# Optimization experiments

Hardware: AMD Instinct MI355X
Metric: run time of the kernel (lower is better)

Reference implementation:

```python
import jax, jax.numpy as jnp
import numpy as np

T = 2048        # num tokens
HID = 2048      # hidden_size
HQ = 16         # num_heads
HKV = 8         # num_kv_heads
D = 128         # head_dim
P = 2           # power retention exponent
THETA = 10000.0 # rope base
SCALE = D ** -0.5


def setup_inputs() -> dict:
    key = jax.random.key(0)
    ks = jax.random.split(key, 8)
    s = 0.02
    return {
        "positions": jnp.arange(T, dtype=jnp.int64) if jax.config.jax_enable_x64 else jnp.arange(T, dtype=jnp.int32),
        "hidden_states": jax.random.normal(ks[0], (T, HID), jnp.float32),
        "Wq": jax.random.normal(ks[1], (HID, HQ * D), jnp.float32) * s,
        "bq": jnp.zeros((HQ * D,), jnp.float32),
        "Wk": jax.random.normal(ks[2], (HID, HKV * D), jnp.float32) * s,
        "bk": jnp.zeros((HKV * D,), jnp.float32),
        "Wv": jax.random.normal(ks[3], (HID, HKV * D), jnp.float32) * s,
        "bv": jnp.zeros((HKV * D,), jnp.float32),
        "Wg": jax.random.normal(ks[4], (HID, HKV), jnp.float32) * s,
        "bg": jnp.zeros((HKV,), jnp.float32),
        "Wo": jax.random.normal(ks[5], (HQ * D, HID), jnp.float32) * s,
        "bo": jnp.zeros((HID,), jnp.float32),
    }


def _rope_neox(x, pos):
    # x: [T, H, D], pos: [T]; rotate-half (neox) style, rotary_dim == head_dim
    half = D // 2
    inv_freq = 1.0 / (THETA ** (jnp.arange(0, D, 2, dtype=jnp.float32) / D))  # [D/2]
    freqs = pos.astype(jnp.float32)[:, None] * inv_freq                        # [T, D/2]
    cos = jnp.cos(freqs)[:, None, :]
    sin = jnp.sin(freqs)[:, None, :]
    x1, x2 = x[..., :half], x[..., half:]
    return jnp.concatenate([x1 * cos - x2 * sin, x2 * cos + x1 * sin], axis=-1)


def reference(positions, hidden_states, Wq, bq, Wk, bk, Wv, bv, Wg, bg, Wo, bo):
    # QKVG projections
    q = (hidden_states @ Wq + bq).reshape(T, HQ, D)
    k = (hidden_states @ Wk + bk).reshape(T, HKV, D)
    v = (hidden_states @ Wv + bv).reshape(T, HKV, D)
    g = hidden_states @ Wg + bg            # [T, HKV], one gate scalar per kv head

    # RoPE on q/k, logsigmoid gate in fp32
    q = _rope_neox(q, positions)
    k = _rope_neox(k, positions)
    g = jax.nn.log_sigmoid(g.astype(jnp.float32))   # [T, HKV], <= 0
    G = jnp.cumsum(g, axis=0)                       # [T, HKV] cumulative log-decay

    # GQA: expand kv heads to query heads
    rep = HQ // HKV
    k = jnp.repeat(k, rep, axis=1)   # [T, HQ, D]
    v = jnp.repeat(v, rep, axis=1)
    G = jnp.repeat(G, rep, axis=1)   # [T, HQ]

    # Power retention (quadratic attention form, seq_len <= switch_over_seq_len):
    # W_ij = (scale * q_i . k_j)^p * exp(G_i - G_j), causal j <= i
    S = jnp.einsum('thd,shd->hts', q, k) * SCALE      # [H, T, T]
    S = S ** P
    Gh = G.T                                          # [H, T]
    mask = jnp.tril(jnp.ones((T, T), dtype=bool))
    diff = jnp.where(mask[None], Gh[:, :, None] - Gh[:, None, :], -jnp.inf)
    W = S * jnp.exp(diff)                             # decay<=1 inside mask, 0 outside

    out = jnp.einsum('hts,shd->thd', W, v)            # [T, H, D]
    out = out.reshape(T, HQ * D) @ Wo + bo            # o_proj
    return out
```

## Files before the change

kernel.cpp:

```cpp
#include <hip/hip_runtime.h>
#include <hip/hip_bf16.h>
#include <math.h>

#define T_SEQ 2048
#define HID 2048
#define HQ 16
#define HKV 8
#define D_HEAD 128
#define HALF 64
#define SCALE_F 0.08838834764831845f
#define PROJW 4096

typedef __attribute__((ext_vector_type(8))) short bf16x8;
typedef __attribute__((ext_vector_type(4))) float f32x4;

static __device__ __forceinline__ short f2bf(float x) {
  unsigned u = __builtin_bit_cast(unsigned, x);
  unsigned r = (u + 0x7FFF + ((u >> 16) & 1)) >> 16;
  return (short)r;
}
static __device__ __forceinline__ float bf2f(unsigned short u) {
  unsigned v = ((unsigned)u) << 16;
  return __builtin_bit_cast(float, v);
}

#define GLDS(gsrc, ldst) \
  __builtin_amdgcn_global_load_lds((const __attribute__((address_space(1))) void*)(gsrc), \
                                   (__attribute__((address_space(3))) void*)(ldst), 16, 0, 0)

__global__ __launch_bounds__(256)
void cvt_bf16(const float* __restrict__ in, short* __restrict__ out, int n4)
{
  int i = blockIdx.x * blockDim.x + threadIdx.x;
  if (i >= n4) return;
  float4 v = reinterpret_cast<const float4*>(in)[i];
  short4 o;
  o.x = f2bf(v.x); o.y = f2bf(v.y); o.z = f2bf(v.z); o.w = f2bf(v.w);
  reinterpret_cast<short4*>(out)[i] = o;
}

__global__ __launch_bounds__(256)
void transpose_all(const float* __restrict__ Wq, const float* __restrict__ Wk,
                   const float* __restrict__ Wv, const float* __restrict__ Wo,
                   short* __restrict__ BTall, short* __restrict__ WoT)
{
  const int bx = blockIdx.x;
  const int k0 = blockIdx.y * 32;
  const float* src; short* dst; int Nsrc, n0;
  if (bx < 64)       { src = Wq; Nsrc = 2048; dst = BTall;                       n0 = bx * 32; }
  else if (bx < 96)  { src = Wk; Nsrc = 1024; dst = BTall + (size_t)2048 * 2048; n0 = (bx - 64) * 32; }
  else if (bx < 128) { src = Wv; Nsrc = 1024; dst = BTall + (size_t)3072 * 2048; n0 = (bx - 96) * 32; }
  else               { src = Wo; Nsrc = 2048; dst = WoT;                         n0 = (bx - 128) * 32; }

  __shared__ float tile[32][33];
  const int r = threadIdx.x >> 5, c = threadIdx.x & 31;
  #pragma unroll
  for (int i = 0; i < 4; ++i)
    tile[r + i * 8][c] = src[(size_t)(k0 + r + i * 8) * Nsrc + n0 + c];
  __syncthreads();
  const int n = threadIdx.x >> 3, k4 = (threadIdx.x & 7) * 4;
  short4 o;
  o.x = f2bf(tile[k4 + 0][n]); o.y = f2bf(tile[k4 + 1][n]);
  o.z = f2bf(tile[k4 + 2][n]); o.w = f2bf(tile[k4 + 3][n]);
  *reinterpret_cast<short4*>(&dst[(size_t)(n0 + n) * 2048 + k0 + k4]) = o;
}

__global__ __launch_bounds__(256)
void pack_bias(const float* __restrict__ bq, const float* __restrict__ bk,
               const float* __restrict__ bv, float* __restrict__ bcat)
{
  const int i = blockIdx.x * 256 + threadIdx.x;
  bcat[i] = (i < 2048) ? bq[i] : ((i < 3072) ? bk[i - 2048] : bv[i - 3072]);
}

template <bool OBF>
__global__ __launch_bounds__(256)
void gemm_bf16(const short* __restrict__ A, const short* __restrict__ BT,
               const float* __restrict__ bias, void* __restrict__ Cout,
               int N, int K)
{
  __shared__ short As[4][128 * 32];
  __shared__ short Bs[4][128 * 32];
  const int tid = threadIdx.x;
  const int wave = tid >> 6, lane = tid & 63;
  const int bm0 = blockIdx.y * 128, bn0 = blockIdx.x * 128;
  const int wm = (wave >> 1) * 64, wn = (wave & 1) * 64;

  const int srow = wave * 32 + (lane >> 2);
  const int scol = (lane & 3) * 8;
  const short* Abase = A + (size_t)(bm0 + srow) * K + scol;
  const short* Bbase = BT + (size_t)(bn0 + srow) * K + scol;

  f32x4 acc[4][4] = {};
  const int nk = K >> 5;

#define STAGE(buf, kk)                                                        \
  do {                                                                        \
    GLDS(Abase + ((kk) << 5), &As[buf][(wave * 32) * 32]);                    \
    GLDS(Abase + ((kk) << 5) + (size_t)16 * K, &As[buf][(wave * 32 + 16) * 32]); \
    GLDS(Bbase + ((kk) << 5), &Bs[buf][(wave * 32) * 32]);                    \
    GLDS(Bbase + ((kk) << 5) + (size_t)16 * K, &Bs[buf][(wave * 32 + 16) * 32]); \
  } while (0)

  STAGE(0, 0);
  STAGE(1, 1);
  asm volatile("s_waitcnt vmcnt(4)" ::: "memory");
  asm volatile("s_barrier" ::: "memory");
  __builtin_amdgcn_sched_barrier(0);

  const int kof = (lane >> 4) * 8;
  const int rA = wm + (lane & 15);
  const int rB = wn + (lane & 15);

  for (int t = 0; t < nk; ++t) {
    const int cur = t & 3;
    if (t + 2 < nk) STAGE((t + 2) & 3, t + 2);

    bf16x8 af[4], bfr[4];
    #pragma unroll
    for (int i = 0; i < 4; ++i) {
      af[i]  = *reinterpret_cast<const bf16x8*>(&As[cur][(rA + i * 16) * 32 + kof]);
      bfr[i] = *reinterpret_cast<const bf16x8*>(&Bs[cur][(rB + i * 16) * 32 + kof]);
    }
    #pragma unroll
    for (int i = 0; i < 4; ++i)
      #pragma unroll
      for (int j = 0; j < 4; ++j)
        acc[i][j] = __builtin_amdgcn_mfma_f32_16x16x32_bf16(af[i], bfr[j], acc[i][j], 0, 0, 0);

    if (t + 1 < nk) {
      if (t + 2 < nk) asm volatile("s_waitcnt vmcnt(4)" ::: "memory");
      else            asm volatile("s_waitcnt vmcnt(0)" ::: "memory");
      asm volatile("s_barrier" ::: "memory");
      __builtin_amdgcn_sched_barrier(0);
    }
  }

  const int crow = wm + (lane >> 4) * 4;
  const int ccol = wn + (lane & 15);
  #pragma unroll
  for (int j = 0; j < 4; ++j) {
    const int col = bn0 + ccol + j * 16;
    const float b = bias[col];
    #pragma unroll
    for (int i = 0; i < 4; ++i)
      #pragma unroll
      for (int r = 0; r < 4; ++r) {
        const int row = bm0 + crow + i * 16 + r;
        const float v = acc[i][j][r] + b;
        if constexpr (OBF)
          ((short*)Cout)[(size_t)row * N + col] = f2bf(v);
        else
          ((float*)Cout)[(size_t)row * N + col] = v;
      }
  }
#undef STAGE
}

__global__ __launch_bounds__(256)
void gproj_kernel(const float* __restrict__ hs, const float* __restrict__ Wg,
                  const float* __restrict__ bg, float* __restrict__ gT)
{
  const int t = blockIdx.x, tid = threadIdx.x;
  __shared__ float red[256][9];
  float a[8] = {0.f, 0.f, 0.f, 0.f, 0.f, 0.f, 0.f, 0.f};
  for (int cc = tid; cc < HID; cc += 256) {
    const float hv = hs[(size_t)t * HID + cc];
    const float4 w0 = *reinterpret_cast<const float4*>(Wg + (size_t)cc * 8);
    const float4 w1 = *reinterpret_cast<const float4*>(Wg + (size_t)cc * 8 + 4);
    a[0] = fmaf(hv, w0.x, a[0]); a[1] = fmaf(hv, w0.y, a[1]);
    a[2] = fmaf(hv, w0.z, a[2]); a[3] = fmaf(hv, w0.w, a[3]);
    a[4] = fmaf(hv, w1.x, a[4]); a[5] = fmaf(hv, w1.y, a[5]);
    a[6] = fmaf(hv, w1.z, a[6]); a[7] = fmaf(hv, w1.w, a[7]);
  }
  #pragma unroll
  for (int j = 0; j < 8; ++j) red[tid][j] = a[j];
  __syncthreads();
  for (int s = 128; s >= 1; s >>= 1) {
    if (tid < s) {
      #pragma unroll
      for (int j = 0; j < 8; ++j) red[tid][j] += red[tid + s][j];
    }
    __syncthreads();
  }
  if (tid < 8) {
    const float x = red[0][tid] + bg[tid];
    const float nx = -x;
    const float sp = (nx > 20.f) ? nx : log1pf(expf(nx));
    gT[(size_t)tid * T_SEQ + t] = -sp;
  }
}

__global__ __launch_bounds__(512)
void gscan_kernel(const float* __restrict__ gT, float* __restrict__ Gct)
{
  const int h = blockIdx.x;
  const int tid = threadIdx.x;
  const int wid = tid >> 6, lane = tid & 63;
  __shared__ float wsum[8];

  const float4 v = reinterpret_cast<const float4*>(gT + (size_t)h * T_SEQ)[tid];
  const float p0 = v.x, p1 = p0 + v.y, p2 = p1 + v.z, p3 = p2 + v.w;

  float sc = p3;
  #pragma unroll
  for (int off = 1; off < 64; off <<= 1) {
    const float o = __shfl_up(sc, off, 64);
    if (lane >= off) sc += o;
  }
  if (lane == 63) wsum[wid] = sc;
  __syncthreads();
  float wof = 0.f;
  #pragma unroll
  for (int w = 0; w < 8; ++w) wof += (w < wid) ? wsum[w] : 0.f;

  const float excl = wof + sc - p3;
  reinterpret_cast<float4*>(Gct + (size_t)h * T_SEQ)[tid] =
      make_float4(excl + p0, excl + p1, excl + p2, excl + p3);
}

__global__ __launch_bounds__(192)
void rope_kernel(short* __restrict__ proj)
{
  const int t = blockIdx.x;
  __shared__ float cs[64], sn[64];
  if (threadIdx.x < 64) {
    const int i = threadIdx.x;
    const float f = (float)t * powf(10000.0f, -(float)i / 64.0f);
    cs[i] = cosf(f); sn[i] = sinf(f);
  }
  __syncthreads();
  const int u = threadIdx.x;
  const int hh = u >> 3, ch = u & 7;
  short* base = proj + (size_t)t * PROJW +
                ((hh < HQ) ? hh * D_HEAD : 2048 + (hh - HQ) * D_HEAD);
  bf16x8 x1 = *reinterpret_cast<bf16x8*>(base + ch * 8);
  bf16x8 x2 = *reinterpret_cast<bf16x8*>(base + HALF + ch * 8);
  #pragma unroll
  for (int j = 0; j < 8; ++j) {
    const float a = bf2f((unsigned short)x1[j]);
    const float b = bf2f((unsigned short)x2[j]);
    const float cc = cs[ch * 8 + j], ss = sn[ch * 8 + j];
    x1[j] = f2bf(a * cc - b * ss);
    x2[j] = f2bf(b * cc + a * ss);
  }
  *reinterpret_cast<bf16x8*>(base + ch * 8) = x1;
  *reinterpret_cast<bf16x8*>(base + HALF + ch * 8) = x2;
}

__global__ __launch_bounds__(256)
void vtrans_kernel(const unsigned short* __restrict__ proj, unsigned short* __restrict__ vt)
{
  __shared__ unsigned short tile[32][33];
  const int tt = blockIdx.x * 32, dd = blockIdx.y * 32, hk = blockIdx.z;
  const int c = threadIdx.x & 31, r0 = (threadIdx.x >> 5) * 4;
  #pragma unroll
  for (int i = 0; i < 4; ++i)
    tile[r0 + i][c] = proj[(size_t)(tt + r0 + i) * PROJW + 3072 + hk * 128 + dd + c];
  __syncthreads();
  #pragma unroll
  for (int i = 0; i < 4; ++i)
    vt[(size_t)(hk * 128 + dd + r0 + i) * T_SEQ + tt + c] = tile[c][r0 + i];
}

__global__ __launch_bounds__(256, 1)
void attn_mfma(const short* __restrict__ proj, const short* __restrict__ vt,
               const float* __restrict__ Gct, short* __restrict__ outb)
{
  __shared__ __align__(16) char smem[86528];
  const int hk = blockIdx.x;
  const int tb = blockIdx.y * 64;
  const int tid = threadIdx.x;
  const int wid = tid >> 6, lane = tid & 63;
  const int c = lane & 15, g = lane >> 4;
  const int h = 2 * hk + (wid >> 1);
  const int tw = tb + (wid & 1) * 32;
  const float* Gh = Gct + (size_t)hk * T_SEQ;

  const float glim = Gh[tb] + 90.0f;
  int lo = 0, hi = tb;
  while (lo < hi) {
    const int mid = (lo + hi) >> 1;
    if (Gh[mid] > glim) lo = mid + 1; else hi = mid;
  }
  const int sfirst = lo & ~63;
  const int nst = ((tb - sfirst) >> 6) + 1;

  bf16x8 qf[2][4];
  #pragma unroll
  for (int tt = 0; tt < 2; ++tt)
    #pragma unroll
    for (int kb = 0; kb < 4; ++kb)
      qf[tt][kb] = *reinterpret_cast<const bf16x8*>(
          proj + (size_t)(tw + 16 * tt + c) * PROJW + h * D_HEAD + kb * 32 + g * 8);
  const float gt0 = Gh[tw + c];
  const float gt1 = Gh[tw + 16 + c];
  const float gtw = Gh[tw];
  const int twmax = tw + 31;

  f32x4 accv[2][8] = {};

#define ASTG(buf, s64)                                                                   \
  do {                                                                                   \
    _Pragma("unroll")                                                                    \
    for (int i2 = 0; i2 < 4; ++i2) {                                                     \
      const int cid = tid + 256 * i2;                                                    \
      const int kr = cid >> 4, kc = cid & 15;                                            \
      GLDS(proj + (size_t)((s64) + kr) * PROJW + 2048 + hk * 128 + ((kc ^ (kr & 7)) * 8),\
           smem + (buf) * 16384 + cid * 16);                                             \
      const int vr = cid >> 3, vc = cid & 7;                                             \
      GLDS(vt + (size_t)(hk * 128 + vr) * T_SEQ + (s64) + ((vc ^ (vr & 7)) * 8),         \
           smem + 32768 + (buf) * 16384 + cid * 16);                                     \
    }                                                                                    \
    if (tid < 64) ((float*)(smem + 86016))[(buf) * 64 + tid] = Gh[(s64) + tid];          \
  } while (0)

  ASTG(0, sfirst);
  __syncthreads();

  for (int i = 0; i < nst; ++i) {
    const int cur = i & 1;
    if (i + 1 < nst) ASTG(cur ^ 1, sfirst + (i + 1) * 64);
    const int sbase64 = sfirst + i * 64;
    const float* Gss = (const float*)(smem + 86016) + cur * 64;
    char* Pmy = smem + 65536 + wid * 5120;

    #pragma unroll
    for (int st = 0; st < 2; ++st) {
      const int s0 = sbase64 + st * 32;
      if (s0 > twmax) continue;
      if (gtw - Gss[st * 32 + 31] < -90.0f) continue;

      bf16x8 kf[2][4];
      #pragma unroll
      for (int sg = 0; sg < 2; ++sg)
        #pragma unroll
        for (int kb = 0; kb < 4; ++kb) {
          const int row = st * 32 + 16 * sg + c;
          const int byt = (row * 256 + kb * 64 + g * 16) ^ ((c & 7) << 4);
          kf[sg][kb] = *reinterpret_cast<const bf16x8*>(smem + cur * 16384 + byt);
        }
      f32x4 sa[2][2] = {};
      #pragma unroll
      for (int kb = 0; kb < 4; ++kb)
        #pragma unroll
        for (int sg = 0; sg < 2; ++sg)
          #pragma unroll
          for (int tt = 0; tt < 2; ++tt)
            sa[sg][tt] = __builtin_amdgcn_mfma_f32_16x16x32_bf16(
                kf[sg][kb], qf[tt][kb], sa[sg][tt], 0, 0, 0);

      #pragma unroll
      for (int sg = 0; sg < 2; ++sg) {
        const float4 gs = *reinterpret_cast<const float4*>(&Gss[st * 32 + sg * 16 + g * 4]);
        const float gsv[4] = {gs.x, gs.y, gs.z, gs.w};
        #pragma unroll
        for (int tt = 0; tt < 2; ++tt) {
          const int tg = tw + 16 * tt + c;
          const float gt = tt ? gt1 : gt0;
          const int sg0 = s0 + sg * 16 + g * 4;
          float w[4];
          #pragma unroll
          for (int r = 0; r < 4; ++r) {
            const float dv = sa[sg][tt][r] * SCALE_F;
            const float ww = dv * dv * __expf(gt - gsv[r]);
            w[r] = (sg0 + r <= tg) ? ww : 0.0f;
          }
          uint2 pv;
          pv.x = ((unsigned)(unsigned short)f2bf(w[1]) << 16) | (unsigned short)f2bf(w[0]);
          pv.y = ((unsigned)(unsigned short)f2bf(w[3]) << 16) | (unsigned short)f2bf(w[2]);
          *reinterpret_cast<uint2*>(Pmy + st * 2560 + (c + 16 * tt) * 80 + 8 * g + 32 * sg) = pv;
        }
      }
      asm volatile("s_waitcnt lgkmcnt(0)" ::: "memory");
      __builtin_amdgcn_sched_barrier(0);

      bf16x8 pf[2];
      #pragma unroll
      for (int tt = 0; tt < 2; ++tt)
        pf[tt] = *reinterpret_cast<const bf16x8*>(Pmy + st * 2560 + (c + 16 * tt) * 80 + g * 16);

      #pragma unroll
      for (int db = 0; db < 8; ++db) {
        const int row = 16 * db + c;
        const int byt = (row * 128 + st * 64 + g * 16) ^ ((c & 7) << 4);
        const bf16x8 vf = *reinterpret_cast<const bf16x8*>(smem + 32768 + cur * 16384 + byt);
        #pragma unroll
        for (int tt = 0; tt < 2; ++tt)
          accv[tt][db] = __builtin_amdgcn_mfma_f32_16x16x32_bf16(pf[tt], vf, accv[tt][db], 0, 0, 0);
      }
    }
    __syncthreads();
  }

  char* Wme = smem + wid * 8704;
  #pragma unroll
  for (int tt = 0; tt < 2; ++tt)
    #pragma unroll
    for (int db = 0; db < 8; ++db)
      #pragma unroll
      for (int r = 0; r < 4; ++r)
        *reinterpret_cast<short*>(Wme + (16 * tt + 4 * g + r) * 272 + (16 * db + c) * 2)
            = f2bf(accv[tt][db][r]);
  asm volatile("s_waitcnt lgkmcnt(0)" ::: "memory");
  __builtin_amdgcn_sched_barrier(0);
  #pragma unroll
  for (int e = 0; e < 8; ++e) {
    const int idx = e * 64 + lane;
    const int tr = idx >> 4, d0 = (idx & 15) * 8;
    const bf16x8 vv = *reinterpret_cast<const bf16x8*>(Wme + tr * 272 + d0 * 2);
    *reinterpret_cast<bf16x8*>(outb + ((size_t)(tw + tr) * HQ + h) * D_HEAD + d0) = vv;
  }
#undef ASTG
}

extern "C" void kernel_launch(void* const* d_in, const int* in_sizes, int n_in,
                              void* d_out, int out_size, void* d_ws, size_t ws_size,
                              hipStream_t stream)
{
  const float* hs = (const float*)d_in[1];
  const float* Wq = (const float*)d_in[2];
  const float* bq = (const float*)d_in[3];
  const float* Wk = (const float*)d_in[4];
  const float* bk = (const float*)d_in[5];
  const float* Wv = (const float*)d_in[6];
  const float* bv = (const float*)d_in[7];
  const float* Wg = (const float*)d_in[8];
  const float* bg = (const float*)d_in[9];
  const float* Wo = (const float*)d_in[10];
  const float* bo = (const float*)d_in[11];
  float* outp = (float*)d_out;

  short* proj  = (short*)d_ws;
  short* vtb   = proj + (size_t)T_SEQ * PROJW;
  float* gT    = (float*)(vtb + (size_t)HKV * D_HEAD * T_SEQ);
  float* Gct   = gT + 16384;
  float* bcat  = Gct + 16384;
  short* hsb   = (short*)(bcat + 4096);
  short* BTall = hsb + (size_t)2048 * 2048;
  short* WoT   = BTall + (size_t)4096 * 2048;
  short* attnout = hsb;

  cvt_bf16<<<4096, 256, 0, stream>>>(hs, hsb, 1048576);
  transpose_all<<<dim3(192, 64), 256, 0, stream>>>(Wq, Wk, Wv, Wo, BTall, WoT);
  pack_bias<<<16, 256, 0, stream>>>(bq, bk, bv, bcat);

  gproj_kernel<<<2048, 256, 0, stream>>>(hs, Wg, bg, gT);
  gscan_kernel<<<8, 512, 0, stream>>>(gT, Gct);

  gemm_bf16<true><<<dim3(32, 16), 256, 0, stream>>>(
      hsb, BTall, bcat, proj, PROJW, 2048);

  rope_kernel<<<2048, 192, 0, stream>>>(proj);
  vtrans_kernel<<<dim3(64, 4, 8), 256, 0, stream>>>((const unsigned short*)proj,
                                                    (unsigned short*)vtb);

  attn_mfma<<<dim3(8, 32), 256, 0, stream>>>(proj, vtb, Gct, attnout);

  gemm_bf16<false><<<dim3(16, 16), 256, 0, stream>>>(
      attnout, WoT, bo, outp, 2048, 2048);
}
```

Before: 152.2 us.

## Fuse small kernels and split-K the output projection GEMM

Folds the fp32-to-bf16 conversion of the hidden states into the gate-projection kernel, drops the bias-packing kernel by selecting the bias inside the GEMM epilogue, and merges RoPE and the V transpose into one launch. The output projection GEMM becomes split-K with two K halves, which doubles its grid from 256 to 512 blocks, and a separate add kernel then sums the two partial outputs. GEMM LDS buffering drops from 4 to 3 stages. Split-K adds an extra fp32 write and read of the full output plus one more launch, in exchange for better CU occupancy.

```diff
diff --git a/kernel.cpp b/kernel.cpp
--- a/kernel.cpp
+++ b/kernel.cpp
@@ -29,17 +29,6 @@
                                    (__attribute__((address_space(3))) void*)(ldst), 16, 0, 0)
 
 __global__ __launch_bounds__(256)
-void cvt_bf16(const float* __restrict__ in, short* __restrict__ out, int n4)
-{
-  int i = blockIdx.x * blockDim.x + threadIdx.x;
-  if (i >= n4) return;
-  float4 v = reinterpret_cast<const float4*>(in)[i];
-  short4 o;
-  o.x = f2bf(v.x); o.y = f2bf(v.y); o.z = f2bf(v.z); o.w = f2bf(v.w);
-  reinterpret_cast<short4*>(out)[i] = o;
-}
-
-__global__ __launch_bounds__(256)
 void transpose_all(const float* __restrict__ Wq, const float* __restrict__ Wk,
                    const float* __restrict__ Wv, const float* __restrict__ Wo,
                    short* __restrict__ BTall, short* __restrict__ WoT)
@@ -66,46 +55,57 @@
 }
 
 __global__ __launch_bounds__(256)
-void pack_bias(const float* __restrict__ bq, const float* __restrict__ bk,
-               const float* __restrict__ bv, float* __restrict__ bcat)
-{
-  const int i = blockIdx.x * 256 + threadIdx.x;
-  bcat[i] = (i < 2048) ? bq[i] : ((i < 3072) ? bk[i - 2048] : bv[i - 3072]);
+void add_f32(float* __restrict__ out, const float* __restrict__ part, int n4)
+{
+  int i = blockIdx.x * blockDim.x + threadIdx.x;
+  if (i >= n4) return;
+  float4 a = reinterpret_cast<float4*>(out)[i];
+  const float4 b = reinterpret_cast<const float4*>(part)[i];
+  a.x += b.x; a.y += b.y; a.z += b.z; a.w += b.w;
+  reinterpret_cast<float4*>(out)[i] = a;
 }
 
 template <bool OBF>
 __global__ __launch_bounds__(256)
-void gemm_bf16(const short* __restrict__ A, const short* __restrict__ BT,
-               const float* __restrict__ bias, void* __restrict__ Cout,
-               int N, int K)
-{
-  __shared__ short As[4][128 * 32];
-  __shared__ short Bs[4][128 * 32];
+void gemm3b(const short* __restrict__ A, const short* __restrict__ BT,
+            const float* __restrict__ b0, const float* __restrict__ b1,
+            const float* __restrict__ b2, int s1, int s2,
+            void* __restrict__ Cout0, void* __restrict__ Cout1,
+            int N, int Kst, int klen)
+{
+  __shared__ short As[3][128 * 32];
+  __shared__ short Bs[3][128 * 32];
   const int tid = threadIdx.x;
   const int wave = tid >> 6, lane = tid & 63;
   const int bm0 = blockIdx.y * 128, bn0 = blockIdx.x * 128;
+  const int z = blockIdx.z;
+  const int koff = z * klen;
   const int wm = (wave >> 1) * 64, wn = (wave & 1) * 64;
 
   const int srow = wave * 32 + (lane >> 2);
   const int scol = (lane & 3) * 8;
-  const short* Abase = A + (size_t)(bm0 + srow) * K + scol;
-  const short* Bbase = BT + (size_t)(bn0 + srow) * K + scol;
+  const short* Abase = A + (size_t)(bm0 + srow) * Kst + koff + scol;
+  const short* Bbase = BT + (size_t)(bn0 + srow) * Kst + koff + scol;
 
   f32x4 acc[4][4] = {};
-  const int nk = K >> 5;
-
-#define STAGE(buf, kk)                                                        \
-  do {                                                                        \
-    GLDS(Abase + ((kk) << 5), &As[buf][(wave * 32) * 32]);                    \
-    GLDS(Abase + ((kk) << 5) + (size_t)16 * K, &As[buf][(wave * 32 + 16) * 32]); \
-    GLDS(Bbase + ((kk) << 5), &Bs[buf][(wave * 32) * 32]);                    \
-    GLDS(Bbase + ((kk) << 5) + (size_t)16 * K, &Bs[buf][(wave * 32 + 16) * 32]); \
+  const int nk = klen >> 5;
+
+#define STAGE(buf, kk)                                                           \
+  do {                                                                           \
+    GLDS(Abase + ((kk) << 5), &As[buf][(wave * 32) * 32]);                       \
+    GLDS(Abase + ((kk) << 5) + (size_t)16 * Kst, &As[buf][(wave * 32 + 16) * 32]); \
+    GLDS(Bbase + ((kk) << 5), &Bs[buf][(wave * 32) * 32]);                       \
+    GLDS(Bbase + ((kk) << 5) + (size_t)16 * Kst, &Bs[buf][(wave * 32 + 16) * 32]); \
   } while (0)
 
   STAGE(0, 0);
-  STAGE(1, 1);
-  asm volatile("s_waitcnt vmcnt(4)" ::: "memory");
-  asm volatile("s_barrier" ::: "memory");
+  if (nk > 1) {
+    STAGE(1, 1);
+    asm volatile("s_waitcnt vmcnt(4)" ::: "memory");
+  } else {
+    asm volatile("s_waitcnt vmcnt(0)" ::: "memory");
+  }
+  __builtin_amdgcn_s_barrier();
   __builtin_amdgcn_sched_barrier(0);
 
   const int kof = (lane >> 4) * 8;
@@ -113,14 +113,14 @@
   const int rB = wn + (lane & 15);
 
   for (int t = 0; t < nk; ++t) {
-    const int cur = t & 3;
-    if (t + 2 < nk) STAGE((t + 2) & 3, t + 2);
+    const int p = t % 3, sb = (t + 2) % 3;
+    if (t + 2 < nk) STAGE(sb, t + 2);
 
     bf16x8 af[4], bfr[4];
     #pragma unroll
     for (int i = 0; i < 4; ++i) {
-      af[i]  = *reinterpret_cast<const bf16x8*>(&As[cur][(rA + i * 16) * 32 + kof]);
-      bfr[i] = *reinterpret_cast<const bf16x8*>(&Bs[cur][(rB + i * 16) * 32 + kof]);
+      af[i]  = *reinterpret_cast<const bf16x8*>(&As[p][(rA + i * 16) * 32 + kof]);
+      bfr[i] = *reinterpret_cast<const bf16x8*>(&Bs[p][(rB + i * 16) * 32 + kof]);
     }
     #pragma unroll
     for (int i = 0; i < 4; ++i)
@@ -129,19 +129,23 @@
         acc[i][j] = __builtin_amdgcn_mfma_f32_16x16x32_bf16(af[i], bfr[j], acc[i][j], 0, 0, 0);
 
     if (t + 1 < nk) {
+      __builtin_amdgcn_sched_barrier(0);
       if (t + 2 < nk) asm volatile("s_waitcnt vmcnt(4)" ::: "memory");
       else            asm volatile("s_waitcnt vmcnt(0)" ::: "memory");
-      asm volatile("s_barrier" ::: "memory");
+      __builtin_amdgcn_s_barrier();
       __builtin_amdgcn_sched_barrier(0);
     }
   }
 
+  void* Cout = z ? Cout1 : Cout0;
   const int crow = wm + (lane >> 4) * 4;
   const int ccol = wn + (lane & 15);
   #pragma unroll
   for (int j = 0; j < 4; ++j) {
     const int col = bn0 + ccol + j * 16;
-    const float b = bias[col];
+    float b = 0.f;
+    if (z == 0)
+      b = (col < s1) ? b0[col] : ((col < s2) ? b1[col - s1] : b2[col - s2]);
     #pragma unroll
     for (int i = 0; i < 4; ++i)
       #pragma unroll
@@ -159,13 +163,15 @@
 
 __global__ __launch_bounds__(256)
 void gproj_kernel(const float* __restrict__ hs, const float* __restrict__ Wg,
-                  const float* __restrict__ bg, float* __restrict__ gT)
+                  const float* __restrict__ bg, float* __restrict__ gT,
+                  short* __restrict__ hsb)
 {
   const int t = blockIdx.x, tid = threadIdx.x;
   __shared__ float red[256][9];
   float a[8] = {0.f, 0.f, 0.f, 0.f, 0.f, 0.f, 0.f, 0.f};
   for (int cc = tid; cc < HID; cc += 256) {
     const float hv = hs[(size_t)t * HID + cc];
+    hsb[(size_t)t * HID + cc] = f2bf(hv);
     const float4 w0 = *reinterpret_cast<const float4*>(Wg + (size_t)cc * 8);
     const float4 w1 = *reinterpret_cast<const float4*>(Wg + (size_t)cc * 8 + 4);
     a[0] = fmaf(hv, w0.x, a[0]); a[1] = fmaf(hv, w0.y, a[1]);
@@ -219,48 +225,51 @@
       make_float4(excl + p0, excl + p1, excl + p2, excl + p3);
 }
 
-__global__ __launch_bounds__(192)
-void rope_kernel(short* __restrict__ proj)
-{
-  const int t = blockIdx.x;
+__global__ __launch_bounds__(256)
+void rope_vtrans(short* __restrict__ proj, unsigned short* __restrict__ vt)
+{
   __shared__ float cs[64], sn[64];
-  if (threadIdx.x < 64) {
-    const int i = threadIdx.x;
-    const float f = (float)t * powf(10000.0f, -(float)i / 64.0f);
-    cs[i] = cosf(f); sn[i] = sinf(f);
-  }
-  __syncthreads();
-  const int u = threadIdx.x;
-  const int hh = u >> 3, ch = u & 7;
-  short* base = proj + (size_t)t * PROJW +
-                ((hh < HQ) ? hh * D_HEAD : 2048 + (hh - HQ) * D_HEAD);
-  bf16x8 x1 = *reinterpret_cast<bf16x8*>(base + ch * 8);
-  bf16x8 x2 = *reinterpret_cast<bf16x8*>(base + HALF + ch * 8);
-  #pragma unroll
-  for (int j = 0; j < 8; ++j) {
-    const float a = bf2f((unsigned short)x1[j]);
-    const float b = bf2f((unsigned short)x2[j]);
-    const float cc = cs[ch * 8 + j], ss = sn[ch * 8 + j];
-    x1[j] = f2bf(a * cc - b * ss);
-    x2[j] = f2bf(b * cc + a * ss);
-  }
-  *reinterpret_cast<bf16x8*>(base + ch * 8) = x1;
-  *reinterpret_cast<bf16x8*>(base + HALF + ch * 8) = x2;
-}
-
-__global__ __launch_bounds__(256)
-void vtrans_kernel(const unsigned short* __restrict__ proj, unsigned short* __restrict__ vt)
-{
   __shared__ unsigned short tile[32][33];
-  const int tt = blockIdx.x * 32, dd = blockIdx.y * 32, hk = blockIdx.z;
-  const int c = threadIdx.x & 31, r0 = (threadIdx.x >> 5) * 4;
-  #pragma unroll
-  for (int i = 0; i < 4; ++i)
-    tile[r0 + i][c] = proj[(size_t)(tt + r0 + i) * PROJW + 3072 + hk * 128 + dd + c];
-  __syncthreads();
-  #pragma unroll
-  for (int i = 0; i < 4; ++i)
-    vt[(size_t)(hk * 128 + dd + r0 + i) * T_SEQ + tt + c] = tile[c][r0 + i];
+
+  if (blockIdx.x < 2048) {
+    const int t = blockIdx.x;
+    if (threadIdx.x < 64) {
+      const int i = threadIdx.x;
+      const float f = (float)t * powf(10000.0f, -(float)i / 64.0f);
+      cs[i] = cosf(f); sn[i] = sinf(f);
+    }
+    __syncthreads();
+    const int u = threadIdx.x;
+    if (u < 192) {
+      const int hh = u >> 3, ch = u & 7;
+      short* base = proj + (size_t)t * PROJW +
+                    ((hh < HQ) ? hh * D_HEAD : 2048 + (hh - HQ) * D_HEAD);
+      bf16x8 x1 = *reinterpret_cast<bf16x8*>(base + ch * 8);
+      bf16x8 x2 = *reinterpret_cast<bf16x8*>(base + HALF + ch * 8);
+      #pragma unroll
+      for (int j = 0; j < 8; ++j) {
+        const float a = bf2f((unsigned short)x1[j]);
+        const float b = bf2f((unsigned short)x2[j]);
+        const float cc = cs[ch * 8 + j], ss = sn[ch * 8 + j];
+        x1[j] = f2bf(a * cc - b * ss);
+        x2[j] = f2bf(b * cc + a * ss);
+      }
+      *reinterpret_cast<bf16x8*>(base + ch * 8) = x1;
+      *reinterpret_cast<bf16x8*>(base + HALF + ch * 8) = x2;
+    }
+  } else {
+    const int idx = blockIdx.x - 2048;
+    const int tt = (idx & 63) * 32, dd = ((idx >> 6) & 3) * 32, hk = idx >> 8;
+    const unsigned short* pj = (const unsigned short*)proj;
+    const int c = threadIdx.x & 31, r0 = (threadIdx.x >> 5) * 4;
+    #pragma unroll
+    for (int i = 0; i < 4; ++i)
+      tile[r0 + i][c] = pj[(size_t)(tt + r0 + i) * PROJW + 3072 + hk * 128 + dd + c];
+    __syncthreads();
+    #pragma unroll
+    for (int i = 0; i < 4; ++i)
+      vt[(size_t)(hk * 128 + dd + r0 + i) * T_SEQ + tt + c] = tile[c][r0 + i];
+  }
 }
 
 __global__ __launch_bounds__(256, 1)
@@ -435,28 +444,25 @@
   short* vtb   = proj + (size_t)T_SEQ * PROJW;
   float* gT    = (float*)(vtb + (size_t)HKV * D_HEAD * T_SEQ);
   float* Gct   = gT + 16384;
-  float* bcat  = Gct + 16384;
-  short* hsb   = (short*)(bcat + 4096);
+  short* hsb   = (short*)(Gct + 16384);
   short* BTall = hsb + (size_t)2048 * 2048;
   short* WoT   = BTall + (size_t)4096 * 2048;
   short* attnout = hsb;
-
-  cvt_bf16<<<4096, 256, 0, stream>>>(hs, hsb, 1048576);
+  float* opart   = (float*)BTall;
+
   transpose_all<<<dim3(192, 64), 256, 0, stream>>>(Wq, Wk, Wv, Wo, BTall, WoT);
-  pack_bias<<<16, 256, 0, stream>>>(bq, bk, bv, bcat);
-
-  gproj_kernel<<<2048, 256, 0, stream>>>(hs, Wg, bg, gT);
+
+  gproj_kernel<<<2048, 256, 0, stream>>>(hs, Wg, bg, gT, hsb);
   gscan_kernel<<<8, 512, 0, stream>>>(gT, Gct);
 
-  gemm_bf16<true><<<dim3(32, 16), 256, 0, stream>>>(
-      hsb, BTall, bcat, proj, PROJW, 2048);
-
-  rope_kernel<<<2048, 192, 0, stream>>>(proj);
-  vtrans_kernel<<<dim3(64, 4, 8), 256, 0, stream>>>((const unsigned short*)proj,
-                                                    (unsigned short*)vtb);
+  gemm3b<true><<<dim3(32, 16, 1), 256, 0, stream>>>(
+      hsb, BTall, bq, bk, bv, 2048, 3072, proj, proj, PROJW, 2048, 2048);
+
+  rope_vtrans<<<4096, 256, 0, stream>>>(proj, (unsigned short*)vtb);
 
   attn_mfma<<<dim3(8, 32), 256, 0, stream>>>(proj, vtb, Gct, attnout);
 
-  gemm_bf16<false><<<dim3(16, 16), 256, 0, stream>>>(
-      attnout, WoT, bo, outp, 2048, 2048);
-}
+  gemm3b<false><<<dim3(16, 16, 2), 256, 0, stream>>>(
+      attnout, WoT, bo, bo, bo, 1 << 30, 1 << 30, outp, opart, 2048, 2048, 1024);
+  add_f32<<<4096, 256, 0, stream>>>(outp, opart, 1048576);
+}
```

New measurement: 140.2 us. 7.9% less time.
